# Kernel tuning notes

Measured on AMD Instinct MI355X. Metric: run time of the kernel, lower is better.

Reference implementation:

```python
import jax, jax.numpy as jnp
import numpy as np

N = 50000      # num_nodes
E = 12500      # num hyperedges
NNZ = 400000   # incidence pairs
OBS = 64
LAT = 64
STEPS = 20     # (t1 - t0) / dt = 1.0 / 0.05
DT = 0.05
SQRT_DT = DT ** 0.5
SIGMA_INIT = 0.1


def setup_inputs() -> dict:
    key = jax.random.key(0)
    ks = jax.random.split(key, 12)
    w = lambda k, o, i: jax.random.normal(k, (o, i), dtype=jnp.float32) * (1.0 / np.sqrt(i))
    return {
        "x": jax.random.normal(ks[0], (N, OBS), dtype=jnp.float32),
        "enc_w1": w(ks[1], LAT, OBS),
        "enc_b1": jnp.zeros((LAT,), jnp.float32),
        "enc_w2": w(ks[2], LAT, LAT),
        "enc_b2": jnp.zeros((LAT,), jnp.float32),
        "conv_w": w(ks[3], LAT, LAT),
        "conv_b": jnp.zeros((LAT,), jnp.float32),
        "sigma": SIGMA_INIT * jnp.ones((LAT,), jnp.float32),
        "dec_w1": w(ks[4], LAT, LAT),
        "dec_b1": jnp.zeros((LAT,), jnp.float32),
        "dec_w2": w(ks[5], OBS, LAT),
        "dec_b2": jnp.zeros((OBS,), jnp.float32),
        "node_idx": jax.random.randint(ks[6], (NNZ,), 0, N),
        "edge_idx": jax.random.randint(ks[7], (NNZ,), 0, E),
        "seed": 0,
    }


def _mlp(x, w1, b1, w2, b2):
    # eqx.nn.MLP depth=1: linear -> relu -> linear, applied per node (vmapped == matmul)
    return jax.nn.relu(x @ w1.T + b1) @ w2.T + b2


def reference(x, enc_w1, enc_b1, enc_w2, enc_b2, conv_w, conv_b, sigma,
              dec_w1, dec_b1, dec_w2, dec_b2, node_idx, edge_idx, seed):
    # incidence degree normalization (HGNN-style), computed once
    ones = jnp.ones((NNZ,), jnp.float32)
    edge_deg_inv = 1.0 / jnp.maximum(jax.ops.segment_sum(ones, edge_idx, num_segments=E), 1.0)
    node_deg_inv = 1.0 / jnp.maximum(jax.ops.segment_sum(ones, node_idx, num_segments=N), 1.0)

    def conv(y):
        m = y @ conv_w.T                                                    # [N, LAT]
        e = jax.ops.segment_sum(m[node_idx], edge_idx, num_segments=E)     # node -> hyperedge
        e = e * edge_deg_inv[:, None]
        out = jax.ops.segment_sum(e[edge_idx], node_idx, num_segments=N)   # hyperedge -> node
        return out * node_deg_inv[:, None] + conv_b

    def step(y, k):
        dw = jax.random.normal(k, (N, LAT), dtype=y.dtype)
        drift = jnp.tanh(conv(y))                       # activation(conv) drift
        y = y + drift * DT + sigma * SQRT_DT * dw       # Euler-Maruyama, diagonal noise
        return y, None

    z0 = _mlp(x, enc_w1, enc_b1, enc_w2, enc_b2)        # encode (n, obs) -> (n, lat)
    keys = jax.random.split(jax.random.key(seed), STEPS)
    z1, _ = jax.lax.scan(step, z0, keys)
    return _mlp(z1, dec_w1, dec_b1, dec_w2, dec_b2)     # decode at t1
```

## Files before the change

### kernel.cpp

```cpp
#include <hip/hip_runtime.h>
#include <stdint.h>

#define N_NODES 50000
#define N_EDGES 12500
#define NNZV    400000
#define STEPS   20
#define DT_F    0.05f
#define SQRTDT_F 0.22360679774997896f

__device__ __forceinline__ float rdlf(float v, int l) {
  return __uint_as_float(__builtin_amdgcn_readlane(__float_as_uint(v), (unsigned)l));
}
__device__ __forceinline__ int rfl(int v) {
  return (int)__builtin_amdgcn_readfirstlane((unsigned)v);
}

__device__ __forceinline__ void tf2x32(uint32_t k0, uint32_t k1,
                                       uint32_t x0, uint32_t x1,
                                       uint32_t& o0, uint32_t& o1) {
  uint32_t k2 = k0 ^ k1 ^ 0x1BD11BDAu;
#define TFR(r) { x0 += x1; x1 = (x1 << (r)) | (x1 >> (32 - (r))); x1 ^= x0; }
  x0 += k0; x1 += k1;
  TFR(13) TFR(15) TFR(26) TFR(6)   x0 += k1; x1 += k2 + 1u;
  TFR(17) TFR(29) TFR(16) TFR(24)  x0 += k2; x1 += k0 + 2u;
  TFR(13) TFR(15) TFR(26) TFR(6)   x0 += k0; x1 += k1 + 3u;
  TFR(17) TFR(29) TFR(16) TFR(24)  x0 += k1; x1 += k2 + 4u;
  TFR(13) TFR(15) TFR(26) TFR(6)   x0 += k2; x1 += k0 + 5u;
#undef TFR
  o0 = x0; o1 = x1;
}

__device__ __forceinline__ float erfinv_fast(float x) {
  float w = -__logf((1.0f - x) * (1.0f + x));
  float p;
  if (w < 5.0f) {
    w = w - 2.5f;
    p =              2.81022636e-08f;
    p = fmaf(p, w,   3.43273939e-07f);
    p = fmaf(p, w,  -3.5233877e-06f);
    p = fmaf(p, w,  -4.39150654e-06f);
    p = fmaf(p, w,   0.00021858087f);
    p = fmaf(p, w,  -0.00125372503f);
    p = fmaf(p, w,  -0.00417768164f);
    p = fmaf(p, w,   0.246640727f);
    p = fmaf(p, w,   1.50140941f);
  } else {
    w = sqrtf(w) - 3.0f;
    p =             -0.000200214257f;
    p = fmaf(p, w,   0.000100950558f);
    p = fmaf(p, w,   0.00134934322f);
    p = fmaf(p, w,  -0.00367342844f);
    p = fmaf(p, w,   0.00573950773f);
    p = fmaf(p, w,  -0.0076224613f);
    p = fmaf(p, w,   0.00943887047f);
    p = fmaf(p, w,   1.00167406f);
    p = fmaf(p, w,   2.83297682f);
  }
  return p * x;
}

__device__ __forceinline__ float bits_to_normal(uint32_t b) {
  float f = __uint_as_float((b >> 9) | 0x3f800000u) - 1.0f;
  const float lo = -0.99999994f;
  float u = fmaf(f, 2.0f, lo);
  u = fmaxf(u, lo);
  return 1.41421356237f * erfinv_fast(u);
}

__device__ __forceinline__ float fast_tanhf(float x) {
  float t = __expf(2.0f * x);
  return 1.0f - 2.0f / (t + 1.0f);
}

__global__ void k_keys(const int* __restrict__ seed, unsigned* __restrict__ keys) {
  int j = threadIdx.x;
  if (j < STEPS) {
    unsigned s = (unsigned)seed[0];
    unsigned o0, o1;
    tf2x32(0u, s, 0u, (unsigned)j, o0, o1);
    keys[2 * j] = o0; keys[2 * j + 1] = o1;
  }
}

__global__ void k_zero(int* __restrict__ p, int n) {
  int i = blockIdx.x * 256 + threadIdx.x;
  if (i < n) p[i] = 0;
}

__global__ void k_hist(const int* __restrict__ nidx, const int* __restrict__ eidx,
                       int* __restrict__ ecnt, int* __restrict__ ncnt) {
  int i = blockIdx.x * 256 + threadIdx.x;
  if (i < NNZV) {
    atomicAdd(&ecnt[eidx[i]], 1);
    atomicAdd(&ncnt[nidx[i]], 1);
  }
}

__global__ __launch_bounds__(256) void k_reduce(const int* __restrict__ cnt, int len,
                                                int* __restrict__ bsum) {
  __shared__ int sh[256];
  int b = blockIdx.x, tid = threadIdx.x;
  int base = b * 1024 + tid * 4;
  int s = 0;
#pragma unroll
  for (int j = 0; j < 4; ++j) {
    int i = base + j;
    if (i < len) s += cnt[i];
  }
  sh[tid] = s;
  __syncthreads();
  for (int off = 128; off > 0; off >>= 1) {
    if (tid < off) sh[tid] += sh[tid + off];
    __syncthreads();
  }
  if (tid == 0) bsum[b] = sh[0];
}

__global__ __launch_bounds__(256) void k_scanb(int* __restrict__ bsum, int nb) {
  __shared__ int sh[256];
  int tid = threadIdx.x;
  int v = (tid < nb) ? bsum[tid] : 0;
  sh[tid] = v;
  __syncthreads();
  for (int off = 1; off < 256; off <<= 1) {
    int t = (tid >= off) ? sh[tid - off] : 0;
    __syncthreads();
    sh[tid] += t;
    __syncthreads();
  }
  if (tid < nb) bsum[tid] = sh[tid] - v;
}

__global__ __launch_bounds__(256) void k_scatter(const int* __restrict__ cnt,
                                                 const int* __restrict__ bsum, int len,
                                                 int* __restrict__ start,
                                                 int* __restrict__ fill,
                                                 float* __restrict__ dinv) {
  __shared__ int sh[256];
  int b = blockIdx.x, tid = threadIdx.x;
  int base = b * 1024 + tid * 4;
  int c[4], lex[4];
  int s = 0;
#pragma unroll
  for (int j = 0; j < 4; ++j) {
    int i = base + j;
    c[j] = (i < len) ? cnt[i] : 0;
    lex[j] = s;
    s += c[j];
  }
  sh[tid] = s;
  __syncthreads();
  for (int off = 1; off < 256; off <<= 1) {
    int t = (tid >= off) ? sh[tid - off] : 0;
    __syncthreads();
    sh[tid] += t;
    __syncthreads();
  }
  int off0 = bsum[b] + sh[tid] - s;
#pragma unroll
  for (int j = 0; j < 4; ++j) {
    int i = base + j;
    if (i < len) {
      start[i] = off0 + lex[j];
      fill[i] = 0;
      dinv[i] = 1.0f / (float)(c[j] > 1 ? c[j] : 1);
    }
  }
}

__global__ void k_fill(const int* __restrict__ nidx, const int* __restrict__ eidx,
                       const int* __restrict__ estart, const int* __restrict__ nstart,
                       int* __restrict__ efill, int* __restrict__ nfill,
                       int* __restrict__ emem, int* __restrict__ nmem) {
  int i = blockIdx.x * 256 + threadIdx.x;
  if (i < NNZV) {
    int e = eidx[i], n = nidx[i];
    int pe = atomicAdd(&efill[e], 1);
    emem[estart[e] + pe] = n;
    int pn = atomicAdd(&nfill[n], 1);
    nmem[nstart[n] + pn] = e;
  }
}

__device__ __forceinline__ void stage_swz(const float* __restrict__ w,
                                          float* __restrict__ lds, int tid) {
  for (int idx = tid; idx < 4096; idx += 256) {
    int j = idx >> 6, k = idx & 63;
    lds[k * 64 + (j ^ k)] = w[idx];
  }
}

__device__ __forceinline__ float seg_gather_scalar(const float* __restrict__ rows,
                                                   const int* __restrict__ mem,
                                                   int st, int deg, int lane) {
  float a0 = 0.f, a1 = 0.f, a2 = 0.f, a3 = 0.f;
  int i = 0;
  for (; i + 8 <= deg; i += 8) {
    int d0 = mem[st + i],     d1 = mem[st + i + 1];
    int d2 = mem[st + i + 2], d3 = mem[st + i + 3];
    int d4 = mem[st + i + 4], d5 = mem[st + i + 5];
    int d6 = mem[st + i + 6], d7 = mem[st + i + 7];
    float v0 = rows[(size_t)d0 * 64 + lane], v1 = rows[(size_t)d1 * 64 + lane];
    float v2 = rows[(size_t)d2 * 64 + lane], v3 = rows[(size_t)d3 * 64 + lane];
    float v4 = rows[(size_t)d4 * 64 + lane], v5 = rows[(size_t)d5 * 64 + lane];
    float v6 = rows[(size_t)d6 * 64 + lane], v7 = rows[(size_t)d7 * 64 + lane];
    a0 += v0 + v1; a1 += v2 + v3; a2 += v4 + v5; a3 += v6 + v7;
  }
  for (; i < deg; ++i)
    a0 += rows[(size_t)mem[st + i] * 64 + lane];
  return (a0 + a1) + (a2 + a3);
}

__global__ __launch_bounds__(256) void k_encoder(
    const float* __restrict__ x, const float* __restrict__ w1,
    const float* __restrict__ b1, const float* __restrict__ w2,
    const float* __restrict__ b2, float* __restrict__ y) {
  __shared__ float lw1[4096], lw2[4096];
  int tid = threadIdx.x;
  stage_swz(w1, lw1, tid);
  stage_swz(w2, lw2, tid);
  __syncthreads();
  int lane = tid & 63, wave = tid >> 6;
  float w1r[64], w2r[64];
#pragma unroll
  for (int k = 0; k < 64; ++k) {
    w1r[k] = lw1[k * 64 + (lane ^ k)];
    w2r[k] = lw2[k * 64 + (lane ^ k)];
  }
  float b1v = b1[lane], b2v = b2[lane];
  int gw = blockIdx.x * 4 + wave, nw = gridDim.x * 4;
  for (int n = gw; n < N_NODES; n += nw) {
    float xv = x[(size_t)n * 64 + lane];
    float a0 = 0.f, a1 = 0.f, a2 = 0.f, a3 = 0.f;
#pragma unroll
    for (int k = 0; k < 64; k += 4) {
      a0 = fmaf(rdlf(xv, k),     w1r[k],     a0);
      a1 = fmaf(rdlf(xv, k + 1), w1r[k + 1], a1);
      a2 = fmaf(rdlf(xv, k + 2), w1r[k + 2], a2);
      a3 = fmaf(rdlf(xv, k + 3), w1r[k + 3], a3);
    }
    float h = fmaxf((a0 + a1) + (a2 + a3) + b1v, 0.f);
    a0 = a1 = a2 = a3 = 0.f;
#pragma unroll
    for (int k = 0; k < 64; k += 4) {
      a0 = fmaf(rdlf(h, k),     w2r[k],     a0);
      a1 = fmaf(rdlf(h, k + 1), w2r[k + 1], a1);
      a2 = fmaf(rdlf(h, k + 2), w2r[k + 2], a2);
      a3 = fmaf(rdlf(h, k + 3), w2r[k + 3], a3);
    }
    y[(size_t)n * 64 + lane] = (a0 + a1) + (a2 + a3) + b2v;
  }
}

__global__ __launch_bounds__(256) void k_edge(
    const float* __restrict__ y, float* __restrict__ e,
    const int* __restrict__ estart, const int* __restrict__ ecnt,
    const int* __restrict__ emem, const float* __restrict__ edinv,
    const float* __restrict__ cw) {
  __shared__ float lcw[4096];
  int tid = threadIdx.x;
  stage_swz(cw, lcw, tid);
  __syncthreads();
  int lane = tid & 63, wave = tid >> 6;
  int gw = blockIdx.x * 4 + wave, nw = gridDim.x * 4;
  for (int ed = gw; ed < N_EDGES; ed += nw) {
    int edu = rfl(ed);
    int st  = estart[edu], deg = ecnt[edu];
    float div = edinv[edu];
    float acc = seg_gather_scalar(y, emem, st, deg, lane);
    float a0 = 0.f, a1 = 0.f, a2 = 0.f, a3 = 0.f;
#pragma unroll
    for (int k = 0; k < 64; k += 4) {
      a0 = fmaf(rdlf(acc, k),     lcw[k * 64 + (lane ^ k)],             a0);
      a1 = fmaf(rdlf(acc, k + 1), lcw[(k + 1) * 64 + (lane ^ (k + 1))], a1);
      a2 = fmaf(rdlf(acc, k + 2), lcw[(k + 2) * 64 + (lane ^ (k + 2))], a2);
      a3 = fmaf(rdlf(acc, k + 3), lcw[(k + 3) * 64 + (lane ^ (k + 3))], a3);
    }
    e[(size_t)edu * 64 + lane] = ((a0 + a1) + (a2 + a3)) * div;
  }
}

__global__ __launch_bounds__(256) void k_node(
    const float* __restrict__ e, float* __restrict__ y,
    const int* __restrict__ nstart, const int* __restrict__ ncnt,
    const int* __restrict__ nmem, const float* __restrict__ ndinv,
    const float* __restrict__ cb, const float* __restrict__ sigma,
    const unsigned* __restrict__ keys, int s) {
  int tid = threadIdx.x;
  int lane = tid & 63, wave = tid >> 6;
  float cbv = cb[lane];
  float sgv = sigma[lane] * SQRTDT_F;
  unsigned ka = keys[2 * s], kb = keys[2 * s + 1];
  int gw = blockIdx.x * 4 + wave, nw = gridDim.x * 4;
  for (int n = gw; n < N_NODES; n += nw) {
    int nu = rfl(n);
    int st = nstart[nu], deg = ncnt[nu];
    float dinv = ndinv[nu];
    float yv = y[(size_t)nu * 64 + lane];
    float acc = seg_gather_scalar(e, nmem, st, deg, lane);
    uint32_t r0, r1;
    tf2x32(ka, kb, 0u, (unsigned)(nu * 64 + lane), r0, r1);
    float dw = bits_to_normal(r0 ^ r1);
    yv = fmaf(fast_tanhf(fmaf(acc, dinv, cbv)), DT_F, fmaf(sgv, dw, yv));
    y[(size_t)nu * 64 + lane] = yv;
  }
}

__global__ __launch_bounds__(256) void k_decoder(
    const float* __restrict__ y, const float* __restrict__ w1,
    const float* __restrict__ b1, const float* __restrict__ w2,
    const float* __restrict__ b2, float* __restrict__ out) {
  __shared__ float lw1[4096], lw2[4096];
  int tid = threadIdx.x;
  stage_swz(w1, lw1, tid);
  stage_swz(w2, lw2, tid);
  __syncthreads();
  int lane = tid & 63, wave = tid >> 6;
  float w1r[64], w2r[64];
#pragma unroll
  for (int k = 0; k < 64; ++k) {
    w1r[k] = lw1[k * 64 + (lane ^ k)];
    w2r[k] = lw2[k * 64 + (lane ^ k)];
  }
  float b1v = b1[lane], b2v = b2[lane];
  int gw = blockIdx.x * 4 + wave, nw = gridDim.x * 4;
  for (int n = gw; n < N_NODES; n += nw) {
    float xv = y[(size_t)n * 64 + lane];
    float a0 = 0.f, a1 = 0.f, a2 = 0.f, a3 = 0.f;
#pragma unroll
    for (int k = 0; k < 64; k += 4) {
      a0 = fmaf(rdlf(xv, k),     w1r[k],     a0);
      a1 = fmaf(rdlf(xv, k + 1), w1r[k + 1], a1);
      a2 = fmaf(rdlf(xv, k + 2), w1r[k + 2], a2);
      a3 = fmaf(rdlf(xv, k + 3), w1r[k + 3], a3);
    }
    float h = fmaxf((a0 + a1) + (a2 + a3) + b1v, 0.f);
    a0 = a1 = a2 = a3 = 0.f;
#pragma unroll
    for (int k = 0; k < 64; k += 4) {
      a0 = fmaf(rdlf(h, k),     w2r[k],     a0);
      a1 = fmaf(rdlf(h, k + 1), w2r[k + 1], a1);
      a2 = fmaf(rdlf(h, k + 2), w2r[k + 2], a2);
      a3 = fmaf(rdlf(h, k + 3), w2r[k + 3], a3);
    }
    out[(size_t)n * 64 + lane] = (a0 + a1) + (a2 + a3) + b2v;
  }
}

extern "C" void kernel_launch(void* const* d_in, const int* in_sizes, int n_in,
                              void* d_out, int out_size, void* d_ws, size_t ws_size,
                              hipStream_t stream) {
  (void)in_sizes; (void)n_in; (void)out_size; (void)ws_size;
  const float* x      = (const float*)d_in[0];
  const float* enc_w1 = (const float*)d_in[1];
  const float* enc_b1 = (const float*)d_in[2];
  const float* enc_w2 = (const float*)d_in[3];
  const float* enc_b2 = (const float*)d_in[4];
  const float* conv_w = (const float*)d_in[5];
  const float* conv_b = (const float*)d_in[6];
  const float* sigma  = (const float*)d_in[7];
  const float* dec_w1 = (const float*)d_in[8];
  const float* dec_b1 = (const float*)d_in[9];
  const float* dec_w2 = (const float*)d_in[10];
  const float* dec_b2 = (const float*)d_in[11];
  const int* node_idx = (const int*)d_in[12];
  const int* edge_idx = (const int*)d_in[13];
  const int* seed     = (const int*)d_in[14];

  char* wsb = (char*)d_ws;
  size_t off = 0;
  auto alloc = [&](size_t bytes) -> void* {
    void* p = wsb + off;
    off = (off + bytes + 255) & ~(size_t)255;
    return p;
  };
  float* y        = (float*)alloc((size_t)N_NODES * 64 * 4);
  float* e        = (float*)alloc((size_t)N_EDGES * 64 * 4);
  int* edge_cnt   = (int*)alloc((size_t)N_EDGES * 4);
  int* node_cnt   = (int*)alloc((size_t)N_NODES * 4);
  int* edge_start = (int*)alloc((size_t)N_EDGES * 4);
  int* node_start = (int*)alloc((size_t)N_NODES * 4);
  int* edge_fill  = (int*)alloc((size_t)N_EDGES * 4);
  int* node_fill  = (int*)alloc((size_t)N_NODES * 4);
  int* edge_mem   = (int*)alloc((size_t)NNZV * 4);
  int* node_mem   = (int*)alloc((size_t)NNZV * 4);
  float* edinv    = (float*)alloc((size_t)N_EDGES * 4);
  float* ndinv    = (float*)alloc((size_t)N_NODES * 4);
  unsigned* keys  = (unsigned*)alloc(2 * STEPS * 4);
  int* ebsum      = (int*)alloc(256 * 4);
  int* nbsum      = (int*)alloc(256 * 4);

  const int EB = (N_EDGES + 1023) / 1024;
  const int NB = (N_NODES + 1023) / 1024;

  dim3 b256(256);
  hipLaunchKernelGGL(k_keys, dim3(1), dim3(64), 0, stream, seed, keys);
  hipLaunchKernelGGL(k_zero, dim3((N_EDGES + 255) / 256), b256, 0, stream, edge_cnt, N_EDGES);
  hipLaunchKernelGGL(k_zero, dim3((N_NODES + 255) / 256), b256, 0, stream, node_cnt, N_NODES);
  hipLaunchKernelGGL(k_hist, dim3((NNZV + 255) / 256), b256, 0, stream,
                     node_idx, edge_idx, edge_cnt, node_cnt);
  hipLaunchKernelGGL(k_reduce, dim3(EB), b256, 0, stream, edge_cnt, N_EDGES, ebsum);
  hipLaunchKernelGGL(k_reduce, dim3(NB), b256, 0, stream, node_cnt, N_NODES, nbsum);
  hipLaunchKernelGGL(k_scanb, dim3(1), b256, 0, stream, ebsum, EB);
  hipLaunchKernelGGL(k_scanb, dim3(1), b256, 0, stream, nbsum, NB);
  hipLaunchKernelGGL(k_scatter, dim3(EB), b256, 0, stream,
                     edge_cnt, ebsum, N_EDGES, edge_start, edge_fill, edinv);
  hipLaunchKernelGGL(k_scatter, dim3(NB), b256, 0, stream,
                     node_cnt, nbsum, N_NODES, node_start, node_fill, ndinv);
  hipLaunchKernelGGL(k_fill, dim3((NNZV + 255) / 256), b256, 0, stream,
                     node_idx, edge_idx, edge_start, node_start,
                     edge_fill, node_fill, edge_mem, node_mem);
  hipLaunchKernelGGL(k_encoder, dim3(1024), b256, 0, stream,
                     x, enc_w1, enc_b1, enc_w2, enc_b2, y);
  for (int s = 0; s < STEPS; ++s) {
    hipLaunchKernelGGL(k_edge, dim3(2048), b256, 0, stream,
                       y, e, edge_start, edge_cnt, edge_mem, edinv, conv_w);
    hipLaunchKernelGGL(k_node, dim3(2048), b256, 0, stream,
                       e, y, node_start, node_cnt, node_mem, ndinv,
                       conv_b, sigma, keys, s);
  }
  hipLaunchKernelGGL(k_decoder, dim3(1024), b256, 0, stream,
                     y, dec_w1, dec_b1, dec_w2, dec_b2, (float*)d_out);
}
```

Baseline: 1.079 ms.

## Process four segments per wave with float4 gathers and LDS-staged indices

The edge and node kernels now split each wave into four 16-lane groups. Each group handles its own hyperedge or node and gathers rows with float4 loads, instead of one wave per segment reading one float per lane. Neighbor indices are first staged cooperatively into LDS, the edge matvec uses a re-swizzled float4 weight layout, and grid sizes are matched to the new work counts. This targets the latency-bound scalar gather loop and the serial index loads. In exchange it brings load imbalance from max-degree loops across the four groups and four Threefry evaluations per lane.

```diff
diff --git a/kernel.cpp b/kernel.cpp
--- a/kernel.cpp
+++ b/kernel.cpp
@@ -10,9 +10,6 @@
 
 __device__ __forceinline__ float rdlf(float v, int l) {
   return __uint_as_float(__builtin_amdgcn_readlane(__float_as_uint(v), (unsigned)l));
-}
-__device__ __forceinline__ int rfl(int v) {
-  return (int)__builtin_amdgcn_readfirstlane((unsigned)v);
 }
 
 __device__ __forceinline__ void tf2x32(uint32_t k0, uint32_t k1,
@@ -190,27 +187,6 @@
   }
 }
 
-__device__ __forceinline__ float seg_gather_scalar(const float* __restrict__ rows,
-                                                   const int* __restrict__ mem,
-                                                   int st, int deg, int lane) {
-  float a0 = 0.f, a1 = 0.f, a2 = 0.f, a3 = 0.f;
-  int i = 0;
-  for (; i + 8 <= deg; i += 8) {
-    int d0 = mem[st + i],     d1 = mem[st + i + 1];
-    int d2 = mem[st + i + 2], d3 = mem[st + i + 3];
-    int d4 = mem[st + i + 4], d5 = mem[st + i + 5];
-    int d6 = mem[st + i + 6], d7 = mem[st + i + 7];
-    float v0 = rows[(size_t)d0 * 64 + lane], v1 = rows[(size_t)d1 * 64 + lane];
-    float v2 = rows[(size_t)d2 * 64 + lane], v3 = rows[(size_t)d3 * 64 + lane];
-    float v4 = rows[(size_t)d4 * 64 + lane], v5 = rows[(size_t)d5 * 64 + lane];
-    float v6 = rows[(size_t)d6 * 64 + lane], v7 = rows[(size_t)d7 * 64 + lane];
-    a0 += v0 + v1; a1 += v2 + v3; a2 += v4 + v5; a3 += v6 + v7;
-  }
-  for (; i < deg; ++i)
-    a0 += rows[(size_t)mem[st + i] * 64 + lane];
-  return (a0 + a1) + (a2 + a3);
-}
-
 __global__ __launch_bounds__(256) void k_encoder(
     const float* __restrict__ x, const float* __restrict__ w1,
     const float* __restrict__ b1, const float* __restrict__ w2,
@@ -258,25 +234,55 @@
     const int* __restrict__ emem, const float* __restrict__ edinv,
     const float* __restrict__ cw) {
   __shared__ float lcw[4096];
+  __shared__ int   sid[4][4][68];
+  __shared__ float xb[4][4][68];
   int tid = threadIdx.x;
-  stage_swz(cw, lcw, tid);
+  for (int idx = tid; idx < 4096; idx += 256) {
+    int f = idx >> 6, k = idx & 63;
+    lcw[k * 64 + ((((f >> 2) ^ (k & 15)) << 2) | (f & 3))] = cw[idx];
+  }
   __syncthreads();
   int lane = tid & 63, wave = tid >> 6;
+  int sub = lane & 15, q = lane >> 4;
+  const int NQ = N_EDGES / 4;
   int gw = blockIdx.x * 4 + wave, nw = gridDim.x * 4;
-  for (int ed = gw; ed < N_EDGES; ed += nw) {
-    int edu = rfl(ed);
-    int st  = estart[edu], deg = ecnt[edu];
-    float div = edinv[edu];
-    float acc = seg_gather_scalar(y, emem, st, deg, lane);
-    float a0 = 0.f, a1 = 0.f, a2 = 0.f, a3 = 0.f;
-#pragma unroll
-    for (int k = 0; k < 64; k += 4) {
-      a0 = fmaf(rdlf(acc, k),     lcw[k * 64 + (lane ^ k)],             a0);
-      a1 = fmaf(rdlf(acc, k + 1), lcw[(k + 1) * 64 + (lane ^ (k + 1))], a1);
-      a2 = fmaf(rdlf(acc, k + 2), lcw[(k + 2) * 64 + (lane ^ (k + 2))], a2);
-      a3 = fmaf(rdlf(acc, k + 3), lcw[(k + 3) * 64 + (lane ^ (k + 3))], a3);
-    }
-    e[(size_t)edu * 64 + lane] = ((a0 + a1) + (a2 + a3)) * div;
+  for (int p = gw; p < NQ; p += nw) {
+    int ed = p * 4 + q;
+    int st = estart[ed], deg = ecnt[ed];
+    float div = edinv[ed];
+    int m = max(deg, __shfl_xor(deg, 16));
+    m = max(m, __shfl_xor(m, 32));
+    float ax = 0.f, ay = 0.f, az = 0.f, aw = 0.f;
+    for (int base = 0; base < m; base += 64) {
+#pragma unroll
+      for (int j = 0; j < 4; ++j) {
+        int idx = base + sub + j * 16;
+        if (idx < deg) sid[wave][q][sub + j * 16] = emem[st + idx];
+      }
+      int rem = min(64, m - base);
+#pragma unroll 2
+      for (int i = 0; i < rem; ++i) {
+        int id = sid[wave][q][i];
+        if (base + i < deg) {
+          const float4 v = *(const float4*)&y[(size_t)id * 64 + sub * 4];
+          ax += v.x; ay += v.y; az += v.z; aw += v.w;
+        }
+      }
+    }
+    float4 a4; a4.x = ax; a4.y = ay; a4.z = az; a4.w = aw;
+    *(float4*)&xb[wave][q][sub * 4] = a4;
+    float ox = 0.f, oy = 0.f, oz = 0.f, ow = 0.f;
+#pragma unroll
+    for (int k = 0; k < 64; ++k) {
+      float xv = xb[wave][q][k];
+      const float4 wv = *(const float4*)&lcw[k * 64 + ((sub ^ (k & 15)) << 2)];
+      ox = fmaf(xv, wv.x, ox);
+      oy = fmaf(xv, wv.y, oy);
+      oz = fmaf(xv, wv.z, oz);
+      ow = fmaf(xv, wv.w, ow);
+    }
+    float4 o4; o4.x = ox * div; o4.y = oy * div; o4.z = oz * div; o4.w = ow * div;
+    *(float4*)&e[(size_t)ed * 64 + sub * 4] = o4;
   }
 }
 
@@ -286,23 +292,51 @@
     const int* __restrict__ nmem, const float* __restrict__ ndinv,
     const float* __restrict__ cb, const float* __restrict__ sigma,
     const unsigned* __restrict__ keys, int s) {
+  __shared__ int sid[4][4][68];
   int tid = threadIdx.x;
   int lane = tid & 63, wave = tid >> 6;
-  float cbv = cb[lane];
-  float sgv = sigma[lane] * SQRTDT_F;
+  int sub = lane & 15, q = lane >> 4;
+  const float4 cb4 = *(const float4*)&cb[sub * 4];
+  float4 sg4 = *(const float4*)&sigma[sub * 4];
+  sg4.x *= SQRTDT_F; sg4.y *= SQRTDT_F; sg4.z *= SQRTDT_F; sg4.w *= SQRTDT_F;
   unsigned ka = keys[2 * s], kb = keys[2 * s + 1];
+  const int NQ = N_NODES / 4;
   int gw = blockIdx.x * 4 + wave, nw = gridDim.x * 4;
-  for (int n = gw; n < N_NODES; n += nw) {
-    int nu = rfl(n);
-    int st = nstart[nu], deg = ncnt[nu];
-    float dinv = ndinv[nu];
-    float yv = y[(size_t)nu * 64 + lane];
-    float acc = seg_gather_scalar(e, nmem, st, deg, lane);
+  for (int p = gw; p < NQ; p += nw) {
+    int n = p * 4 + q;
+    int st = nstart[n], deg = ncnt[n];
+    float dinv = ndinv[n];
+    float4 yv = *(const float4*)&y[(size_t)n * 64 + sub * 4];
+    int m = max(deg, __shfl_xor(deg, 16));
+    m = max(m, __shfl_xor(m, 32));
+    float ax = 0.f, ay = 0.f, az = 0.f, aw = 0.f;
+    for (int base = 0; base < m; base += 64) {
+#pragma unroll
+      for (int j = 0; j < 4; ++j) {
+        int idx = base + sub + j * 16;
+        if (idx < deg) sid[wave][q][sub + j * 16] = nmem[st + idx];
+      }
+      int rem = min(64, m - base);
+#pragma unroll 2
+      for (int i = 0; i < rem; ++i) {
+        int id = sid[wave][q][i];
+        if (base + i < deg) {
+          const float4 v = *(const float4*)&e[(size_t)id * 64 + sub * 4];
+          ax += v.x; ay += v.y; az += v.z; aw += v.w;
+        }
+      }
+    }
+    unsigned c0 = (unsigned)(n * 64 + sub * 4);
     uint32_t r0, r1;
-    tf2x32(ka, kb, 0u, (unsigned)(nu * 64 + lane), r0, r1);
-    float dw = bits_to_normal(r0 ^ r1);
-    yv = fmaf(fast_tanhf(fmaf(acc, dinv, cbv)), DT_F, fmaf(sgv, dw, yv));
-    y[(size_t)nu * 64 + lane] = yv;
+    tf2x32(ka, kb, 0u, c0 + 0u, r0, r1); float d0 = bits_to_normal(r0 ^ r1);
+    tf2x32(ka, kb, 0u, c0 + 1u, r0, r1); float d1 = bits_to_normal(r0 ^ r1);
+    tf2x32(ka, kb, 0u, c0 + 2u, r0, r1); float d2 = bits_to_normal(r0 ^ r1);
+    tf2x32(ka, kb, 0u, c0 + 3u, r0, r1); float d3 = bits_to_normal(r0 ^ r1);
+    yv.x = fmaf(fast_tanhf(fmaf(ax, dinv, cb4.x)), DT_F, fmaf(sg4.x, d0, yv.x));
+    yv.y = fmaf(fast_tanhf(fmaf(ay, dinv, cb4.y)), DT_F, fmaf(sg4.y, d1, yv.y));
+    yv.z = fmaf(fast_tanhf(fmaf(az, dinv, cb4.z)), DT_F, fmaf(sg4.z, d2, yv.z));
+    yv.w = fmaf(fast_tanhf(fmaf(aw, dinv, cb4.w)), DT_F, fmaf(sg4.w, d3, yv.w));
+    *(float4*)&y[(size_t)n * 64 + sub * 4] = yv;
   }
 }
 
@@ -382,8 +416,8 @@
   int* node_start = (int*)alloc((size_t)N_NODES * 4);
   int* edge_fill  = (int*)alloc((size_t)N_EDGES * 4);
   int* node_fill  = (int*)alloc((size_t)N_NODES * 4);
-  int* edge_mem   = (int*)alloc((size_t)NNZV * 4);
-  int* node_mem   = (int*)alloc((size_t)NNZV * 4);
+  int* edge_mem   = (int*)alloc((size_t)NNZV * 4 + 64);
+  int* node_mem   = (int*)alloc((size_t)NNZV * 4 + 64);
   float* edinv    = (float*)alloc((size_t)N_EDGES * 4);
   float* ndinv    = (float*)alloc((size_t)N_NODES * 4);
   unsigned* keys  = (unsigned*)alloc(2 * STEPS * 4);
@@ -413,9 +447,9 @@
   hipLaunchKernelGGL(k_encoder, dim3(1024), b256, 0, stream,
                      x, enc_w1, enc_b1, enc_w2, enc_b2, y);
   for (int s = 0; s < STEPS; ++s) {
-    hipLaunchKernelGGL(k_edge, dim3(2048), b256, 0, stream,
+    hipLaunchKernelGGL(k_edge, dim3(782), b256, 0, stream,
                        y, e, edge_start, edge_cnt, edge_mem, edinv, conv_w);
-    hipLaunchKernelGGL(k_node, dim3(2048), b256, 0, stream,
+    hipLaunchKernelGGL(k_node, dim3(3125), b256, 0, stream,
                        e, y, node_start, node_cnt, node_mem, ndinv,
                        conv_b, sigma, keys, s);
   }
```

New measurement: 2.019 ms. 1.87x slower.
